# Performance work log

Hardware: AMD Instinct MI355X
Metric: run time of the kernel (lower is better)

Reference implementation:

```python
import jax, jax.numpy as jnp
import numpy as np

B = 8192
NUM_NETS, N_NODES, NUM_OUT, DIM_OUT = 30, 20, 10, 16
NUM_ITER = 3
IN_DIM = 28 * 28


def squash(t, axis=-1):
    # scale * t / ||t||, scale = ||t||^2 / (1 + ||t||^2)
    sq = jnp.sum(t * t, axis=axis, keepdims=True)
    return (sq / (1.0 + sq)) * t / jnp.sqrt(sq)


def setup_inputs() -> dict:
    key = jax.random.key(0)
    ks = jax.random.split(key, 6)
    return {
        "x": jax.random.normal(ks[0], (B, IN_DIM), dtype=jnp.float32),
        "W1": jax.random.normal(ks[1], (NUM_NETS, IN_DIM, N_NODES), dtype=jnp.float32) * 0.05,
        "b1": jax.random.normal(ks[2], (NUM_NETS, N_NODES), dtype=jnp.float32) * 0.05,
        "W2": jax.random.normal(ks[3], (NUM_NETS, N_NODES, N_NODES), dtype=jnp.float32) * 0.05,
        "b2": jax.random.normal(ks[4], (NUM_NETS, N_NODES), dtype=jnp.float32) * 0.05,
        "route_weights": jax.random.normal(ks[5], (NUM_OUT, NUM_NETS, N_NODES, DIM_OUT), dtype=jnp.float32),
    }


def reference(x, W1, b1, W2, b2, route_weights):
    # 30 independent MLPs batched into one grouped GEMM each
    h = jax.nn.relu(jnp.einsum("bi,nio->bno", x, W1) + b1)          # [B,N,20]
    h = jax.nn.relu(jnp.einsum("bnd,nde->bne", h, W2) + b2)          # [B,N,20]
    u = squash(h, axis=-1)                                            # per-net squash over features
    # priors[b,o,n,k] = sum_d u[b,n,d] * route_weights[o,n,d,k]
    priors = jnp.einsum("bnd,ondk->bonk", u, route_weights)          # [B,O,N,K]
    # logits are constant along K in the original; keep [B,O,N,1] (exact math)
    logits = jnp.zeros(priors.shape[:3] + (1,), dtype=priors.dtype)
    v = None
    for i in range(NUM_ITER):
        probs = jax.nn.softmax(logits, axis=1)                        # over output capsules
        v = squash(jnp.sum(probs * priors, axis=2, keepdims=True))    # [B,O,1,K]
        if i != NUM_ITER - 1:
            logits = logits + jnp.sum(priors * v, axis=-1, keepdims=True)
    return jnp.squeeze(v, axis=2)                                     # [B,O,K]
```

## Files before the change

### kernel.cpp

```cpp
#include <hip/hip_runtime.h>


typedef unsigned short bfu;
typedef unsigned int u32;
typedef __attribute__((ext_vector_type(8))) short short8;
typedef __attribute__((ext_vector_type(4))) float floatx4;

__device__ __forceinline__ float bf2f(bfu u) { union { u32 i; float f; } v; v.i = ((u32)u) << 16; return v.f; }
__device__ __forceinline__ float lo2f(u32 w) { union { u32 i; float f; } v; v.i = w << 16; return v.f; }
__device__ __forceinline__ float hi2f(u32 w) { union { u32 i; float f; } v; v.i = w & 0xffff0000u; return v.f; }
__device__ __forceinline__ float ldf(const void* p, int idx, bool b16) {
    return b16 ? bf2f(((const bfu*)p)[idx]) : ((const float*)p)[idx];
}
__device__ __forceinline__ bfu f2bf(float f) {
    u32 u = __float_as_uint(f);
    return (bfu)((u + 0x7FFFu + ((u >> 16) & 1u)) >> 16);
}
__device__ __forceinline__ void unpack8(uint4 q, float* dst) {
    dst[0] = lo2f(q.x); dst[1] = hi2f(q.x);
    dst[2] = lo2f(q.y); dst[3] = hi2f(q.y);
    dst[4] = lo2f(q.z); dst[5] = hi2f(q.z);
    dst[6] = lo2f(q.w); dst[7] = hi2f(q.w);
}
__device__ __forceinline__ u32 detect_one(const u32* p) {
    int c = 0;
    for (int i = 0; i < 64; i++) {
        u32 e = (p[i] >> 7) & 0xFF;
        c += (e >= 64 && e <= 140) ? 1 : 0;
    }
    return (c >= 48) ? 1u : 0u;
}

__global__ void prep_all(const void* x, const void* W1, const void* b1,
                         const void* W2, const void* b2, const void* rw,
                         bfu* __restrict__ xb, bfu* __restrict__ Wt,
                         float* __restrict__ b1f, bfu* __restrict__ rwb,
                         bfu* __restrict__ rwn, float* __restrict__ W2t,
                         float* __restrict__ b2f,
                         u32* __restrict__ flags_g, int B, int mode) {
    __shared__ u32 flg[6];
    {
        const int t = threadIdx.x;
        if (t < 6) {
            const u32* p = (t == 0) ? (const u32*)x : (t == 1) ? (const u32*)W1
                         : (t == 2) ? (const u32*)b1 : (t == 3) ? (const u32*)W2
                         : (t == 4) ? (const u32*)b2 : (const u32*)rw;
            flg[t] = detect_one(p);
        }
    }
    __syncthreads();
    if (blockIdx.x == 0 && threadIdx.x < 6) flags_g[threadIdx.x] = flg[threadIdx.x];

    const int idx = blockIdx.x * 256 + threadIdx.x;
    const int nxb4 = B * 200;
    if (idx < nxb4) {
        const bool b16 = flg[0] != 0;
        int b = idx / 200, kk = (idx - b * 200) * 4;
        ushort4 w;
        if (kk < 784) {
            int src = b * 784 + kk;
            if (b16) {
                w = *(const ushort4*)((const bfu*)x + src);
            } else {
                float4 f = *(const float4*)((const float*)x + src);
                w.x = f2bf(f.x); w.y = f2bf(f.y); w.z = f2bf(f.z); w.w = f2bf(f.w);
            }
        } else { w.x = 0; w.y = 0; w.z = 0; w.w = 0; }
        *(ushort4*)(xb + b * 800 + kk) = w;
        return;
    }
    int i2 = idx - nxb4;
    if (i2 < 128000) {
        const bool wb = flg[1] != 0;
        int c = i2 / 200, k = (i2 - c * 200) * 4;
        ushort4 w; w.x = 0; w.y = 0; w.z = 0; w.w = 0;
        if (c < 600 && k < 784) {
            int nn = c / 20, o = c - nn * 20;
            int src = nn * 15680 + k * 20 + o;
            if (wb) {
                const bfu* p = (const bfu*)W1;
                w.x = p[src]; w.y = p[src + 20]; w.z = p[src + 40]; w.w = p[src + 60];
            } else {
                const float* p = (const float*)W1;
                w.x = f2bf(p[src]); w.y = f2bf(p[src + 20]);
                w.z = f2bf(p[src + 40]); w.w = f2bf(p[src + 60]);
            }
        }
        *(ushort4*)(Wt + c * 800 + k) = w;
        return;
    }
    i2 -= 128000;
    if (i2 < 640) {
        b1f[i2] = (i2 < 600) ? ldf(b1, i2, flg[2] != 0) : 0.f;
        return;
    }
    i2 -= 640;
    if (mode == 0) {
        if (i2 < 153600) {
            const bool rb = flg[5] != 0;
            int dd = i2 % 32;
            int col = (i2 / 32) % 160;
            int n = i2 / 5120;
            bfu v = 0;
            if (dd < 20) {
                int o = col / 16, kk = col % 16;
                int src = o * 9600 + n * 320 + dd * 16 + kk;
                v = rb ? ((const bfu*)rw)[src] : f2bf(((const float*)rw)[src]);
            }
            rwn[i2] = v;
            return;
        }
        i2 -= 153600;
        if (i2 < 12000) {
            int d = i2 % 20;
            int e = (i2 / 20) % 20;
            int n = i2 / 400;
            W2t[i2] = ldf(W2, n * 400 + d * 20 + e, flg[3] != 0);
            return;
        }
        i2 -= 12000;
        if (i2 < 640) {
            b2f[i2] = (i2 < 600) ? ldf(b2, i2, flg[4] != 0) : 0.f;
        }
    } else {
        if (i2 < 96000) {
            const bool rb = flg[5] != 0;
            int d = i2 % 20;
            int k = (i2 / 20) % 16;
            int n = (i2 / 320) % 30;
            int o = i2 / 9600;
            int src = o * 9600 + n * 320 + d * 16 + k;
            rwb[i2] = rb ? ((const bfu*)rw)[src] : f2bf(((const float*)rw)[src]);
        }
    }
}

__global__ __launch_bounds__(256, 4) void k1m(const bfu* __restrict__ xb, const bfu* __restrict__ Wt,
                                              const float* __restrict__ b1f,
                                              float* __restrict__ h1, int Btot, int tr) {
    __shared__ __align__(16) char smem[128 * 68 * 4];
    short* As = (short*)smem;
    short* Bs = (short*)(smem + 128 * 72 * 2);
    const int tid = threadIdx.x;
    const int w = tid >> 6, lane = tid & 63;
    const int quad = lane >> 4, fl = lane & 15;
    const int m0 = blockIdx.x * 128, n0 = blockIdx.y * 64;

    floatx4 acc[2][4];
    #pragma unroll
    for (int mi = 0; mi < 2; mi++)
        #pragma unroll
        for (int ni = 0; ni < 4; ni++) acc[mi][ni] = (floatx4){0.f, 0.f, 0.f, 0.f};

    const int arow = tid >> 1, aseg = tid & 1;
    const int brow = tid >> 2, bseg = tid & 3;
    int agrow = m0 + arow; if (agrow >= Btot) agrow = Btot - 1;
    const bfu* abase = xb + (size_t)agrow * 800 + aseg * 32;
    const bfu* bbase = Wt + (size_t)(n0 + brow) * 800 + bseg * 16;

    for (int k0 = 0; k0 < 768; k0 += 64) {
        uint4 qa0 = *(const uint4*)(abase + k0);
        uint4 qa1 = *(const uint4*)(abase + k0 + 8);
        uint4 qa2 = *(const uint4*)(abase + k0 + 16);
        uint4 qa3 = *(const uint4*)(abase + k0 + 24);
        uint4 qb0 = *(const uint4*)(bbase + k0);
        uint4 qb1 = *(const uint4*)(bbase + k0 + 8);

        __syncthreads();
        *(uint4*)&As[arow * 72 + aseg * 32 + 0]  = qa0;
        *(uint4*)&As[arow * 72 + aseg * 32 + 8]  = qa1;
        *(uint4*)&As[arow * 72 + aseg * 32 + 16] = qa2;
        *(uint4*)&As[arow * 72 + aseg * 32 + 24] = qa3;
        *(uint4*)&Bs[brow * 72 + bseg * 16 + 0]  = qb0;
        *(uint4*)&Bs[brow * 72 + bseg * 16 + 8]  = qb1;
        __syncthreads();

        short8 af[2][2], bfr[4][2];
        #pragma unroll
        for (int mi = 0; mi < 2; mi++)
            #pragma unroll
            for (int kk = 0; kk < 2; kk++)
                af[mi][kk] = *(const short8*)&As[(w * 32 + mi * 16 + fl) * 72 + kk * 32 + quad * 8];
        #pragma unroll
        for (int ni = 0; ni < 4; ni++)
            #pragma unroll
            for (int kk = 0; kk < 2; kk++)
                bfr[ni][kk] = *(const short8*)&Bs[(ni * 16 + fl) * 72 + kk * 32 + quad * 8];
        #pragma unroll
        for (int kk = 0; kk < 2; kk++)
            #pragma unroll
            for (int mi = 0; mi < 2; mi++)
                #pragma unroll
                for (int ni = 0; ni < 4; ni++)
                    acc[mi][ni] = __builtin_amdgcn_mfma_f32_16x16x32_bf16(af[mi][kk], bfr[ni][kk], acc[mi][ni], 0, 0, 0);
    }

    {
        const bfu* at = xb + (size_t)agrow * 800 + 768 + aseg * 16;
        const bfu* bt = Wt + (size_t)(n0 + brow) * 800 + 768 + bseg * 8;
        uint4 qa0 = *(const uint4*)(at);
        uint4 qa1 = *(const uint4*)(at + 8);
        uint4 qb0 = *(const uint4*)(bt);

        __syncthreads();
        *(uint4*)&As[arow * 72 + aseg * 16 + 0] = qa0;
        *(uint4*)&As[arow * 72 + aseg * 16 + 8] = qa1;
        *(uint4*)&Bs[brow * 72 + bseg * 8] = qb0;
        __syncthreads();

        short8 af[2], bfr[4];
        #pragma unroll
        for (int mi = 0; mi < 2; mi++)
            af[mi] = *(const short8*)&As[(w * 32 + mi * 16 + fl) * 72 + quad * 8];
        #pragma unroll
        for (int ni = 0; ni < 4; ni++)
            bfr[ni] = *(const short8*)&Bs[(ni * 16 + fl) * 72 + quad * 8];
        #pragma unroll
        for (int mi = 0; mi < 2; mi++)
            #pragma unroll
            for (int ni = 0; ni < 4; ni++)
                acc[mi][ni] = __builtin_amdgcn_mfma_f32_16x16x32_bf16(af[mi], bfr[ni], acc[mi][ni], 0, 0, 0);
    }

    if (tr) {
        __syncthreads();
        float* ep = (float*)smem;
        #pragma unroll
        for (int mi = 0; mi < 2; mi++) {
            #pragma unroll
            for (int ni = 0; ni < 4; ni++) {
                const int c = n0 + ni * 16 + fl;
                const float bias = b1f[c];
                #pragma unroll
                for (int r = 0; r < 4; r++)
                    ep[(w * 32 + mi * 16 + quad * 4 + r) * 68 + ni * 16 + fl]
                        = fmaxf(acc[mi][ni][r] + bias, 0.f);
            }
        }
        __syncthreads();
        #pragma unroll
        for (int s = 0; s < 8; s++) {
            const int i = s * 256 + tid;
            const int ml = i >> 4, cq = i & 15;
            const int c = n0 + cq * 4;
            const int m = m0 + ml;
            if (c < 600 && m < Btot) {
                const int cn = c / 20, ce = c - cn * 20;
                *(float4*)(h1 + ((size_t)cn * Btot + m) * 20 + ce)
                    = *(const float4*)&ep[ml * 68 + cq * 4];
            }
        }
    } else {
        #pragma unroll
        for (int mi = 0; mi < 2; mi++) {
            #pragma unroll
            for (int ni = 0; ni < 4; ni++) {
                const int c = n0 + ni * 16 + fl;
                #pragma unroll
                for (int r = 0; r < 4; r++) {
                    const int m = m0 + w * 32 + mi * 16 + quad * 4 + r;
                    if (c < 600 && m < Btot)
                        h1[(size_t)m * 600 + c] = fmaxf(acc[mi][ni][r] + b1f[c], 0.f);
                }
            }
        }
    }
}

__global__ __launch_bounds__(256) void k2w(const float* __restrict__ h1n,
                                           const float* __restrict__ W2t,
                                           const float* __restrict__ b2f,
                                           const bfu* __restrict__ rwn,
                                           bfu* __restrict__ pri, int Btot) {
    __shared__ short us[128 * 40];
    __shared__ short pst[64 * 168];
    const int tid = threadIdx.x;
    const int n = blockIdx.y;
    const int b0 = blockIdx.x * 128;

    const int w = tid >> 6, lane = tid & 63;
    const int quad = lane >> 4, fl = lane & 15;
    short8 bfr[10];
    #pragma unroll
    for (int nj = 0; nj < 10; nj++)
        bfr[nj] = *(const short8*)(rwn + ((size_t)n * 160 + nj * 16 + fl) * 32 + quad * 8);

    {
        const int row = tid >> 1, half = tid & 1;
        int br = b0 + row; if (br >= Btot) br = Btot - 1;
        float h[20];
        const float* hp = h1n + ((size_t)n * Btot + br) * 20;
        #pragma unroll
        for (int d4 = 0; d4 < 20; d4 += 4) {
            float4 v = *(const float4*)(hp + d4);
            h[d4] = v.x; h[d4 + 1] = v.y; h[d4 + 2] = v.z; h[d4 + 3] = v.w;
        }
        const float* wn = W2t + n * 400;
        const float* bn = b2f + n * 20;
        float o[10], sq = 0.f;
        #pragma unroll
        for (int i = 0; i < 10; i++) {
            const int e = 2 * i + half;
            float acc = bn[e];
            #pragma unroll
            for (int d = 0; d < 20; d++) acc += h[d] * wn[e * 20 + d];
            acc = fmaxf(acc, 0.f);
            o[i] = acc;
            sq += acc * acc;
        }
        sq += __shfl_xor(sq, 1);
        float sc = (sq > 0.f) ? sqrtf(sq) / (1.f + sq) : 0.f;
        #pragma unroll
        for (int i = 0; i < 10; i++)
            us[row * 40 + 2 * i + half] = (short)f2bf(o[i] * sc);
        #pragma unroll
        for (int i = 10; i < 16; i++)
            us[row * 40 + 2 * i + half] = 0;
    }
    __syncthreads();

    #pragma unroll
    for (int mi = 0; mi < 2; mi++) {
        short8 af = *(const short8*)&us[(w * 32 + mi * 16 + fl) * 40 + quad * 8];
        #pragma unroll
        for (int nj = 0; nj < 10; nj++) {
            floatx4 acc = (floatx4){0.f, 0.f, 0.f, 0.f};
            acc = __builtin_amdgcn_mfma_f32_16x16x32_bf16(af, bfr[nj], acc, 0, 0, 0);
            #pragma unroll
            for (int r = 0; r < 4; r++)
                pst[(w * 16 + quad * 4 + r) * 168 + nj * 16 + fl] = (short)f2bf(acc[r]);
        }
        __syncthreads();
        #pragma unroll
        for (int s = 0; s < 5; s++) {
            int i = s * 256 + tid;
            int rl = i / 20, seg = i - rl * 20;
            int row = b0 + (rl >> 4) * 32 + mi * 16 + (rl & 15);
            if (row < Btot)
                *(uint4*)(pri + (size_t)row * 4800 + n * 160 + seg * 8)
                    = *(const uint4*)&pst[rl * 168 + seg * 8];
        }
        __syncthreads();
    }
}

__device__ __forceinline__ void k2_core(const float* hp, const float* wn, const float* bn,
                                        float* o, float& sc) {
    float h[20];
    #pragma unroll
    for (int d4 = 0; d4 < 20; d4 += 4) {
        float4 v = *(const float4*)(hp + d4);
        h[d4] = v.x; h[d4 + 1] = v.y; h[d4 + 2] = v.z; h[d4 + 3] = v.w;
    }
    float sq = 0.f;
    #pragma unroll
    for (int e = 0; e < 20; e++) {
        float acc = bn[e];
        #pragma unroll
        for (int d = 0; d < 20; d++) acc += h[d] * wn[d * 20 + e];
        acc = fmaxf(acc, 0.f);
        o[e] = acc;
        sq += acc * acc;
    }
    sc = (sq > 0.f) ? sqrtf(sq) / (1.f + sq) : 0.f;
}

__global__ __launch_bounds__(256) void k2s(const float* h1, const void* W2, const void* b2,
                                           float* u, const u32* flags, int total) {
    __shared__ float W2s[12000];
    __shared__ float b2s[600];
    const bool wb = flags[3] != 0, bb = flags[4] != 0;
    const int tid = threadIdx.x;
    for (int i = tid; i < 12000; i += 256) W2s[i] = ldf(W2, i, wb);
    for (int i = tid; i < 600; i += 256) b2s[i] = ldf(b2, i, bb);
    __syncthreads();

    int t = blockIdx.x * 256 + tid;
    if (t >= total) return;
    const int b = t / 30, n = t - b * 30;
    float o[20], sc;
    k2_core(h1 + (size_t)b * 600 + n * 20, &W2s[n * 400], &b2s[n * 20], o, sc);
    float* up = u + (size_t)b * 600 + n * 20;
    #pragma unroll
    for (int e4 = 0; e4 < 20; e4 += 4) {
        float4 v;
        v.x = o[e4] * sc; v.y = o[e4 + 1] * sc; v.z = o[e4 + 2] * sc; v.w = o[e4 + 3] * sc;
        *(float4*)(up + e4) = v;
    }
}

__global__ __launch_bounds__(320, 4) void k3w(const bfu* __restrict__ pri_buf,
                                              float* __restrict__ out, int Btot) {
    __shared__ float L[2][300];
    __shared__ float P[2][300];
    __shared__ float S[2][200];
    const int tid = threadIdx.x;
    const int g = tid / 160, r = tid - g * 160;
    const int o = r >> 4, j = r & 15;
    const int b0 = blockIdx.x * 2;
    int bb = b0 + g; if (bb >= Btot) bb = Btot - 1;

    const int n0 = 2 * j, n1 = n0 + 1;
    float p0[16], p1[16];
    if (j < 15) {
        const bfu* pb = pri_buf + (size_t)bb * 4800 + n0 * 160 + o * 16;
        uint4 q0 = *(const uint4*)(pb);
        uint4 q1 = *(const uint4*)(pb + 8);
        uint4 q2 = *(const uint4*)(pb + 160);
        uint4 q3 = *(const uint4*)(pb + 168);
        unpack8(q0, p0); unpack8(q1, p0 + 8);
        unpack8(q2, p1); unpack8(q3, p1 + 8);
    } else {
        #pragma unroll
        for (int i = 0; i < 16; i++) { p0[i] = 0.f; p1[i] = 0.f; }
    }

    float L0 = 0.f, L1 = 0.f;
    float v = 0.f;
    #pragma unroll
    for (int it = 0; it < 3; it++) {
        float P0, P1;
        if (it == 0) {
            P0 = 0.1f; P1 = 0.1f;
        } else {
            if (r < 30) {
                float l[10];
                #pragma unroll
                for (int oo = 0; oo < 10; oo++) l[oo] = L[g][r * 10 + oo];
                float mx = l[0];
                #pragma unroll
                for (int oo = 1; oo < 10; oo++) mx = fmaxf(mx, l[oo]);
                float den = 0.f;
                #pragma unroll
                for (int oo = 0; oo < 10; oo++) { l[oo] = __expf(l[oo] - mx); den += l[oo]; }
                float inv = 1.f / den;
                #pragma unroll
                for (int oo = 0; oo < 10; oo++) P[g][r * 10 + oo] = l[oo] * inv;
            }
            __syncthreads();
            P0 = (j < 15) ? P[g][n0 * 10 + o] : 0.f;
            P1 = (j < 15) ? P[g][n1 * 10 + o] : 0.f;
        }

        float t[16];
        #pragma unroll
        for (int i = 0; i < 16; i++) t[i] = P0 * p0[i] + P1 * p1[i];

        #pragma unroll
        for (int i = 0; i < 8; i++) {
            float send = (j & 8) ? t[i] : t[i + 8];
            float recv = __shfl_xor(send, 8, 16);
            t[i] = ((j & 8) ? t[i + 8] : t[i]) + recv;
        }
        #pragma unroll
        for (int i = 0; i < 4; i++) {
            float send = (j & 4) ? t[i] : t[i + 4];
            float recv = __shfl_xor(send, 4, 16);
            t[i] = ((j & 4) ? t[i + 4] : t[i]) + recv;
        }
        #pragma unroll
        for (int i = 0; i < 2; i++) {
            float send = (j & 2) ? t[i] : t[i + 2];
            float recv = __shfl_xor(send, 2, 16);
            t[i] = ((j & 2) ? t[i + 2] : t[i]) + recv;
        }
        {
            float send = (j & 1) ? t[0] : t[1];
            float recv = __shfl_xor(send, 1, 16);
            t[0] = ((j & 1) ? t[1] : t[0]) + recv;
        }
        float s = t[0];

        if (it < 2) {
            S[g][o * 20 + j] = s;
            float4 s0 = *(const float4*)&S[g][o * 20 + 0];
            float4 s1 = *(const float4*)&S[g][o * 20 + 4];
            float4 s2 = *(const float4*)&S[g][o * 20 + 8];
            float4 s3 = *(const float4*)&S[g][o * 20 + 12];
            float sf[16];
            sf[0] = s0.x;  sf[1] = s0.y;  sf[2] = s0.z;  sf[3] = s0.w;
            sf[4] = s1.x;  sf[5] = s1.y;  sf[6] = s1.z;  sf[7] = s1.w;
            sf[8] = s2.x;  sf[9] = s2.y;  sf[10] = s2.z; sf[11] = s2.w;
            sf[12] = s3.x; sf[13] = s3.y; sf[14] = s3.z; sf[15] = s3.w;
            float q = 0.f;
            #pragma unroll
            for (int k = 0; k < 16; k++) q += sf[k] * sf[k];
            float scale = sqrtf(q) / (1.f + q);
            v = s * scale;
            float d0 = 0.f, d1 = 0.f;
            #pragma unroll
            for (int k = 0; k < 16; k++) {
                float vk = sf[k] * scale;
                d0 += p0[k] * vk;
                d1 += p1[k] * vk;
            }
            L0 += d0; L1 += d1;
            if (j < 15) {
                L[g][n0 * 10 + o] = L0;
                L[g][n1 * 10 + o] = L1;
            }
            __syncthreads();
        } else {
            float q = s * s;
            q += __shfl_xor(q, 1, 16);
            q += __shfl_xor(q, 2, 16);
            q += __shfl_xor(q, 4, 16);
            q += __shfl_xor(q, 8, 16);
            v = s * sqrtf(q) / (1.f + q);
        }
    }
    if ((b0 + g) < Btot) out[(size_t)(b0 + g) * 160 + r] = v;
}

__global__ __launch_bounds__(640, 2) void k3y2(const float* __restrict__ u,
                                               const bfu* __restrict__ rwb,
                                               float* __restrict__ out, int Btot) {
    __shared__ float US[4][600];
    __shared__ float L[4][300];
    __shared__ float P[4][300];
    const int tid = threadIdx.x;
    const int g = tid / 160, r = tid - g * 160;
    const int o = r >> 4, k = r & 15;
    const int b0 = blockIdx.x * 4;

    {
        const int nf4 = 150;
        for (int i = tid; i < 4 * nf4; i += 640) {
            int gg = i / nf4, j = i - gg * nf4;
            int bb = b0 + gg; if (bb >= Btot) bb = Btot - 1;
            *(float4*)&US[gg][j * 4] = *(const float4*)(u + (size_t)bb * 600 + j * 4);
        }
        for (int i = tid; i < 1200; i += 640) L[i / 300][i % 300] = 0.f;
    }
    __syncthreads();

    float pri[30];
    const bfu* rp = rwb + o * 9600 + k * 20;
    #pragma unroll 2
    for (int n = 0; n < 30; n++) {
        const uint2* rq = (const uint2*)(rp + n * 320);
        float a = 0.f;
        #pragma unroll
        for (int jj = 0; jj < 5; jj++) {
            uint2 w = rq[jj];
            float4 uu = *(const float4*)&US[g][n * 20 + jj * 4];
            a += lo2f(w.x) * uu.x + hi2f(w.x) * uu.y + lo2f(w.y) * uu.z + hi2f(w.y) * uu.w;
        }
        pri[n] = a;
    }

    float v = 0.f;
    for (int it = 0; it < 3; it++) {
        if (r < 30) {
            const int n = r;
            float mx = L[g][n * 10];
            #pragma unroll
            for (int oo = 1; oo < 10; oo++) mx = fmaxf(mx, L[g][n * 10 + oo]);
            float e[10], den = 0.f;
            #pragma unroll
            for (int oo = 0; oo < 10; oo++) { e[oo] = __expf(L[g][n * 10 + oo] - mx); den += e[oo]; }
            float inv = 1.f / den;
            #pragma unroll
            for (int oo = 0; oo < 10; oo++) P[g][n * 10 + oo] = e[oo] * inv;
        }
        __syncthreads();
        float s = 0.f;
        #pragma unroll
        for (int n = 0; n < 30; n++) s += P[g][n * 10 + o] * pri[n];
        float q = s * s;
        q += __shfl_xor(q, 1, 16);
        q += __shfl_xor(q, 2, 16);
        q += __shfl_xor(q, 4, 16);
        q += __shfl_xor(q, 8, 16);
        v = s * sqrtf(q) / (1.f + q);
        if (it < 2) {
            #pragma unroll 5
            for (int n = 0; n < 30; n++) {
                float t = pri[n] * v;
                t += __shfl_xor(t, 1, 16);
                t += __shfl_xor(t, 2, 16);
                t += __shfl_xor(t, 4, 16);
                t += __shfl_xor(t, 8, 16);
                if (k == 0) L[g][n * 10 + o] += t;
            }
            __syncthreads();
        }
    }
    if ((b0 + g) < Btot) out[(size_t)(b0 + g) * 160 + r] = v;
}

extern "C" void kernel_launch(void* const* d_in, const int* in_sizes, int n_in,
                              void* d_out, int out_size, void* d_ws, size_t ws_size,
                              hipStream_t stream) {
    int ix = -1, iw1 = -1, ib1 = -1, iw2 = -1, ib2 = -1, irw = -1;
    for (int i = 0; i < n_in; i++) {
        int s = in_sizes[i];
        if (s == 470400 && iw1 < 0) iw1 = i;
        else if (s == 12000 && iw2 < 0) iw2 = i;
        else if (s == 96000 && irw < 0) irw = i;
        else if (s == 600) { if (ib1 < 0) ib1 = i; else if (ib2 < 0) ib2 = i; }
    }
    long bestsz = -1;
    for (int i = 0; i < n_in; i++) {
        if (i == iw1 || i == iw2 || i == irw || i == ib1 || i == ib2) continue;
        if ((long)in_sizes[i] > bestsz) { bestsz = in_sizes[i]; ix = i; }
    }
    if (ix < 0 || iw1 < 0 || ib1 < 0 || iw2 < 0 || ib2 < 0 || irw < 0) {
        ix = 0; iw1 = 1; ib1 = 2; iw2 = 3; ib2 = 4; irw = 5;
    }
    const void* x  = d_in[ix];
    const void* W1 = d_in[iw1];
    const void* b1 = d_in[ib1];
    const void* W2 = d_in[iw2];
    const void* b2 = d_in[ib2];
    const void* rw = d_in[irw];
    const int B = in_sizes[ix] / 784;
    float* out = (float*)d_out;

    char* base = (char*)d_ws;
    size_t off = 0;
    float* h1u  = (float*)(base + off); off += (size_t)B * 2400;
    float* b1f  = (float*)(base + off); off += 2560;
    u32*  flags = (u32*)(base + off);   off += 32;
    bfu*   Wt   = (bfu*)(base + off);   off += 1024000;
    bfu*   xb   = (bfu*)(base + off);   off += (size_t)B * 1600;
    bfu*   rwb  = (bfu*)(base + off);   off += 192000;
    size_t fb_bytes = off;
    bfu*   rwn  = (bfu*)(base + off);   off += 307200;
    float* W2t  = (float*)(base + off); off += 48000;
    float* b2f  = (float*)(base + off); off += 2560;
    bfu*   pri  = (bfu*)(base + off);   off += (size_t)B * 9600;
    size_t main_bytes = off;

    const int mode = (ws_size >= main_bytes) ? 0 : 1;
    const int prep_total = B * 200 + 128000 + 640
                         + (mode == 0 ? (153600 + 12000 + 640) : 96000);

    prep_all<<<(prep_total + 255) / 256, 256, 0, stream>>>(x, W1, b1, W2, b2, rw,
                                                           xb, Wt, b1f, rwb, rwn,
                                                           W2t, b2f, flags, B, mode);
    k1m<<<dim3((B + 127) / 128, 10), 256, 0, stream>>>(xb, Wt, b1f, h1u, B, mode == 0 ? 1 : 0);
    if (mode == 0) {
        k2w<<<dim3((B + 127) / 128, 30), 256, 0, stream>>>(h1u, W2t, b2f, rwn, pri, B);
        k3w<<<(B + 1) / 2, 320, 0, stream>>>(pri, out, B);
    } else {
        (void)fb_bytes;
        k2s<<<(B * 30 + 255) / 256, 256, 0, stream>>>(h1u, W2, b2, h1u, flags, B * 30);
        k3y2<<<(B + 3) / 4, 640, 0, stream>>>(h1u, rwb, out, B);
    }
}
```

Measured before the change: 163.3 us.

## Narrow layer-1 GEMM N-tile, hoist k2w activation loads, raise occupancy bounds

The first GEMM kernel drops its N tile from 64 to 32 columns, so the grid grows from 10 to 19 column blocks. Shared memory and accumulators shrink, and launch bounds go up to 6 blocks per CU, aiming for more waves in flight and better fill across CUs. The k2w kernel now issues its activation loads before the route-weight fragment loads so the latencies overlap. k3w's minimum blocks per CU hint is raised to 8. In exchange, the x tile is re-read from global memory about twice as often, and the tighter register budget may cause spills.

```diff
diff --git a/kernel.cpp b/kernel.cpp
--- a/kernel.cpp
+++ b/kernel.cpp
@@ -135,28 +135,28 @@
     }
 }
 
-__global__ __launch_bounds__(256, 4) void k1m(const bfu* __restrict__ xb, const bfu* __restrict__ Wt,
+__global__ __launch_bounds__(256, 6) void k1p(const bfu* __restrict__ xb, const bfu* __restrict__ Wt,
                                               const float* __restrict__ b1f,
                                               float* __restrict__ h1, int Btot, int tr) {
-    __shared__ __align__(16) char smem[128 * 68 * 4];
+    __shared__ __align__(16) char smem[23040];
     short* As = (short*)smem;
     short* Bs = (short*)(smem + 128 * 72 * 2);
     const int tid = threadIdx.x;
     const int w = tid >> 6, lane = tid & 63;
     const int quad = lane >> 4, fl = lane & 15;
-    const int m0 = blockIdx.x * 128, n0 = blockIdx.y * 64;
-
-    floatx4 acc[2][4];
+    const int m0 = blockIdx.x * 128, n0 = blockIdx.y * 32;
+
+    floatx4 acc[2][2];
     #pragma unroll
     for (int mi = 0; mi < 2; mi++)
         #pragma unroll
-        for (int ni = 0; ni < 4; ni++) acc[mi][ni] = (floatx4){0.f, 0.f, 0.f, 0.f};
+        for (int ni = 0; ni < 2; ni++) acc[mi][ni] = (floatx4){0.f, 0.f, 0.f, 0.f};
 
     const int arow = tid >> 1, aseg = tid & 1;
-    const int brow = tid >> 2, bseg = tid & 3;
+    const int brow = tid >> 3, bseg = tid & 7;
     int agrow = m0 + arow; if (agrow >= Btot) agrow = Btot - 1;
     const bfu* abase = xb + (size_t)agrow * 800 + aseg * 32;
-    const bfu* bbase = Wt + (size_t)(n0 + brow) * 800 + bseg * 16;
+    const bfu* bbase = Wt + (size_t)(n0 + brow) * 800 + bseg * 8;
 
     for (int k0 = 0; k0 < 768; k0 += 64) {
         uint4 qa0 = *(const uint4*)(abase + k0);
@@ -164,25 +164,23 @@
         uint4 qa2 = *(const uint4*)(abase + k0 + 16);
         uint4 qa3 = *(const uint4*)(abase + k0 + 24);
         uint4 qb0 = *(const uint4*)(bbase + k0);
-        uint4 qb1 = *(const uint4*)(bbase + k0 + 8);
 
         __syncthreads();
         *(uint4*)&As[arow * 72 + aseg * 32 + 0]  = qa0;
         *(uint4*)&As[arow * 72 + aseg * 32 + 8]  = qa1;
         *(uint4*)&As[arow * 72 + aseg * 32 + 16] = qa2;
         *(uint4*)&As[arow * 72 + aseg * 32 + 24] = qa3;
-        *(uint4*)&Bs[brow * 72 + bseg * 16 + 0]  = qb0;
-        *(uint4*)&Bs[brow * 72 + bseg * 16 + 8]  = qb1;
-        __syncthreads();
-
-        short8 af[2][2], bfr[4][2];
+        *(uint4*)&Bs[brow * 72 + bseg * 8] = qb0;
+        __syncthreads();
+
+        short8 af[2][2], bfr[2][2];
         #pragma unroll
         for (int mi = 0; mi < 2; mi++)
             #pragma unroll
             for (int kk = 0; kk < 2; kk++)
                 af[mi][kk] = *(const short8*)&As[(w * 32 + mi * 16 + fl) * 72 + kk * 32 + quad * 8];
         #pragma unroll
-        for (int ni = 0; ni < 4; ni++)
+        for (int ni = 0; ni < 2; ni++)
             #pragma unroll
             for (int kk = 0; kk < 2; kk++)
                 bfr[ni][kk] = *(const short8*)&Bs[(ni * 16 + fl) * 72 + kk * 32 + quad * 8];
@@ -191,34 +189,34 @@
             #pragma unroll
             for (int mi = 0; mi < 2; mi++)
                 #pragma unroll
-                for (int ni = 0; ni < 4; ni++)
+                for (int ni = 0; ni < 2; ni++)
                     acc[mi][ni] = __builtin_amdgcn_mfma_f32_16x16x32_bf16(af[mi][kk], bfr[ni][kk], acc[mi][ni], 0, 0, 0);
     }
 
     {
         const bfu* at = xb + (size_t)agrow * 800 + 768 + aseg * 16;
-        const bfu* bt = Wt + (size_t)(n0 + brow) * 800 + 768 + bseg * 8;
         uint4 qa0 = *(const uint4*)(at);
         uint4 qa1 = *(const uint4*)(at + 8);
-        uint4 qb0 = *(const uint4*)(bt);
+        uint4 qb0;
+        if (bseg < 4) qb0 = *(const uint4*)(Wt + (size_t)(n0 + brow) * 800 + 768 + bseg * 8);
 
         __syncthreads();
         *(uint4*)&As[arow * 72 + aseg * 16 + 0] = qa0;
         *(uint4*)&As[arow * 72 + aseg * 16 + 8] = qa1;
-        *(uint4*)&Bs[brow * 72 + bseg * 8] = qb0;
-        __syncthreads();
-
-        short8 af[2], bfr[4];
+        if (bseg < 4) *(uint4*)&Bs[brow * 72 + bseg * 8] = qb0;
+        __syncthreads();
+
+        short8 af[2], bfr[2];
         #pragma unroll
         for (int mi = 0; mi < 2; mi++)
             af[mi] = *(const short8*)&As[(w * 32 + mi * 16 + fl) * 72 + quad * 8];
         #pragma unroll
-        for (int ni = 0; ni < 4; ni++)
+        for (int ni = 0; ni < 2; ni++)
             bfr[ni] = *(const short8*)&Bs[(ni * 16 + fl) * 72 + quad * 8];
         #pragma unroll
         for (int mi = 0; mi < 2; mi++)
             #pragma unroll
-            for (int ni = 0; ni < 4; ni++)
+            for (int ni = 0; ni < 2; ni++)
                 acc[mi][ni] = __builtin_amdgcn_mfma_f32_16x16x32_bf16(af[mi], bfr[ni], acc[mi][ni], 0, 0, 0);
     }
 
@@ -228,33 +226,33 @@
         #pragma unroll
         for (int mi = 0; mi < 2; mi++) {
             #pragma unroll
-            for (int ni = 0; ni < 4; ni++) {
+            for (int ni = 0; ni < 2; ni++) {
                 const int c = n0 + ni * 16 + fl;
                 const float bias = b1f[c];
                 #pragma unroll
                 for (int r = 0; r < 4; r++)
-                    ep[(w * 32 + mi * 16 + quad * 4 + r) * 68 + ni * 16 + fl]
+                    ep[(w * 32 + mi * 16 + quad * 4 + r) * 36 + ni * 16 + fl]
                         = fmaxf(acc[mi][ni][r] + bias, 0.f);
             }
         }
         __syncthreads();
         #pragma unroll
-        for (int s = 0; s < 8; s++) {
+        for (int s = 0; s < 4; s++) {
             const int i = s * 256 + tid;
-            const int ml = i >> 4, cq = i & 15;
+            const int ml = i >> 3, cq = i & 7;
             const int c = n0 + cq * 4;
             const int m = m0 + ml;
             if (c < 600 && m < Btot) {
                 const int cn = c / 20, ce = c - cn * 20;
                 *(float4*)(h1 + ((size_t)cn * Btot + m) * 20 + ce)
-                    = *(const float4*)&ep[ml * 68 + cq * 4];
+                    = *(const float4*)&ep[ml * 36 + cq * 4];
             }
         }
     } else {
         #pragma unroll
         for (int mi = 0; mi < 2; mi++) {
             #pragma unroll
-            for (int ni = 0; ni < 4; ni++) {
+            for (int ni = 0; ni < 2; ni++) {
                 const int c = n0 + ni * 16 + fl;
                 #pragma unroll
                 for (int r = 0; r < 4; r++) {
@@ -280,21 +278,28 @@
 
     const int w = tid >> 6, lane = tid & 63;
     const int quad = lane >> 4, fl = lane & 15;
+
+    const int row = tid >> 1, half = tid & 1;
+    int br = b0 + row; if (br >= Btot) br = Btot - 1;
+    const float* hp = h1n + ((size_t)n * Btot + br) * 20;
+    float4 hv0 = *(const float4*)(hp + 0);
+    float4 hv1 = *(const float4*)(hp + 4);
+    float4 hv2 = *(const float4*)(hp + 8);
+    float4 hv3 = *(const float4*)(hp + 12);
+    float4 hv4 = *(const float4*)(hp + 16);
+
     short8 bfr[10];
     #pragma unroll
     for (int nj = 0; nj < 10; nj++)
         bfr[nj] = *(const short8*)(rwn + ((size_t)n * 160 + nj * 16 + fl) * 32 + quad * 8);
 
     {
-        const int row = tid >> 1, half = tid & 1;
-        int br = b0 + row; if (br >= Btot) br = Btot - 1;
         float h[20];
-        const float* hp = h1n + ((size_t)n * Btot + br) * 20;
-        #pragma unroll
-        for (int d4 = 0; d4 < 20; d4 += 4) {
-            float4 v = *(const float4*)(hp + d4);
-            h[d4] = v.x; h[d4 + 1] = v.y; h[d4 + 2] = v.z; h[d4 + 3] = v.w;
-        }
+        h[0] = hv0.x; h[1] = hv0.y; h[2] = hv0.z; h[3] = hv0.w;
+        h[4] = hv1.x; h[5] = hv1.y; h[6] = hv1.z; h[7] = hv1.w;
+        h[8] = hv2.x; h[9] = hv2.y; h[10] = hv2.z; h[11] = hv2.w;
+        h[12] = hv3.x; h[13] = hv3.y; h[14] = hv3.z; h[15] = hv3.w;
+        h[16] = hv4.x; h[17] = hv4.y; h[18] = hv4.z; h[19] = hv4.w;
         const float* wn = W2t + n * 400;
         const float* bn = b2f + n * 20;
         float o[10], sq = 0.f;
@@ -335,9 +340,9 @@
         for (int s = 0; s < 5; s++) {
             int i = s * 256 + tid;
             int rl = i / 20, seg = i - rl * 20;
-            int row = b0 + (rl >> 4) * 32 + mi * 16 + (rl & 15);
-            if (row < Btot)
-                *(uint4*)(pri + (size_t)row * 4800 + n * 160 + seg * 8)
+            int rw2 = b0 + (rl >> 4) * 32 + mi * 16 + (rl & 15);
+            if (rw2 < Btot)
+                *(uint4*)(pri + (size_t)rw2 * 4800 + n * 160 + seg * 8)
                     = *(const uint4*)&pst[rl * 168 + seg * 8];
         }
         __syncthreads();
@@ -389,7 +394,7 @@
     }
 }
 
-__global__ __launch_bounds__(320, 4) void k3w(const bfu* __restrict__ pri_buf,
+__global__ __launch_bounds__(320, 8) void k3w(const bfu* __restrict__ pri_buf,
                                               float* __restrict__ out, int Btot) {
     __shared__ float L[2][300];
     __shared__ float P[2][300];
@@ -639,7 +644,7 @@
     prep_all<<<(prep_total + 255) / 256, 256, 0, stream>>>(x, W1, b1, W2, b2, rw,
                                                            xb, Wt, b1f, rwb, rwn,
                                                            W2t, b2f, flags, B, mode);
-    k1m<<<dim3((B + 127) / 128, 10), 256, 0, stream>>>(xb, Wt, b1f, h1u, B, mode == 0 ? 1 : 0);
+    k1p<<<dim3((B + 127) / 128, 19), 256, 0, stream>>>(xb, Wt, b1f, h1u, B, mode == 0 ? 1 : 0);
     if (mode == 0) {
         k2w<<<dim3((B + 127) / 128, 30), 256, 0, stream>>>(h1u, W2t, b2f, rwn, pri, B);
         k3w<<<(B + 1) / 2, 320, 0, stream>>>(pri, out, B);
```

New measurement: 170.6 us. +4.5%, slower.
